# Kernel optimization log

Measured on AMD Instinct MI355X. Metric: run time of the kernel, lower is better.

Reference implementation:

```python
import jax, jax.numpy as jnp
import numpy as np

RC = 5.0          # cutoff radius (init arg rc)
N = 4096          # number of atoms
L = 40.0          # cubic box edge; rc <= 0.5*L so MIC branch is valid


def setup_inputs() -> dict:
    key = jax.random.key(0)
    coord = jax.random.uniform(key, (N, 3), dtype=jnp.float32) * L
    cell = L * jnp.eye(3, dtype=jnp.float32)
    return {"coord": coord, "cell": cell}


def reference(coord, cell):
    """MIC neighbor predicate, identical math to the torch cell-list MIC path.

    Returns:
      d2_masked: [n, n] float32, squared distance where pair is a neighbor
                 (0 < dist2 < rc^2), else 0. Row i, col j corresponds to the
                 directed pair (i, j) the torch module would emit in ind_2.
      shift:     [n, n, 3] int32 MIC lattice shift for each kept pair, 0 elsewhere.
    """
    rc2 = jnp.float32(RC * RC)
    H_inv = jnp.linalg.inv(cell)
    frac = coord @ H_inv
    frac = frac - jnp.floor(frac)                    # wrap into [0,1)
    # dfrac[i, j] = frac[j] - frac[i]  (j - i, matching torch: dj_frac - di_frac)
    dfrac = frac[None, :, :] - frac[:, None, :]      # [n, n, 3]
    shift_f = -jnp.round(dfrac)                      # MIC shift (float, in {-1,0,1})
    dfrac = dfrac + shift_f
    d = dfrac @ cell                                 # Cartesian displacement [n, n, 3]
    dist2 = jnp.sum(d * d, axis=-1)                  # [n, n]
    keep = (dist2 > 0.0) & (dist2 < rc2)
    d2_masked = jnp.where(keep, dist2, jnp.float32(0.0))
    shift = jnp.where(keep[..., None], shift_f.astype(jnp.int32), 0)
    return d2_masked, shift
```

## Files before the change

### kernel.cpp

```cpp
#include <hip/hip_runtime.h>


constexpr int N_ATOMS = 4096;
constexpr float RC2 = 25.0f;

typedef float v3f __attribute__((ext_vector_type(3)));

__global__ __launch_bounds__(256) void cellnl_kernel(
    const float* __restrict__ coord,
    const float* __restrict__ cell,
    float* __restrict__ out)
{
    const float L   = cell[0];
    const float inv = 1.0f / L;

    const int i = blockIdx.x >> 4;
    const int j = ((blockIdx.x & 15) << 8) + threadIdx.x;

    float fix = coord[3 * i + 0] * inv; fix -= floorf(fix);
    float fiy = coord[3 * i + 1] * inv; fiy -= floorf(fiy);
    float fiz = coord[3 * i + 2] * inv; fiz -= floorf(fiz);

    const v3f cjv = *reinterpret_cast<const v3f*>(coord + 3 * j);
    float fjx = cjv.x * inv; fjx -= floorf(fjx);
    float fjy = cjv.y * inv; fjy -= floorf(fjy);
    float fjz = cjv.z * inv; fjz -= floorf(fjz);

    float dx = fjx - fix, dy = fjy - fiy, dz = fjz - fiz;
    const float sx = -rintf(dx), sy = -rintf(dy), sz = -rintf(dz);
    dx += sx; dy += sy; dz += sz;
    dx *= L; dy *= L; dz *= L;

    const float dist2 = dx * dx + dy * dy + dz * dz;
    const bool keep = (dist2 > 0.0f) && (dist2 < RC2);

    const size_t p = (size_t)i * N_ATOMS + j;

    out[p] = keep ? dist2 : 0.0f;

    v3f sv;
    sv.x = keep ? sx : 0.0f;
    sv.y = keep ? sy : 0.0f;
    sv.z = keep ? sz : 0.0f;
    *reinterpret_cast<v3f*>(out + (size_t)N_ATOMS * N_ATOMS + p * 3) = sv;
}

extern "C" void kernel_launch(void* const* d_in, const int* in_sizes, int n_in,
                              void* d_out, int out_size, void* d_ws, size_t ws_size,
                              hipStream_t stream) {
    const float* coord = (const float*)d_in[0];
    const float* cell  = (const float*)d_in[1];
    float* out = (float*)d_out;

    const int blocks = N_ATOMS * (N_ATOMS / 256);
    hipLaunchKernelGGL(cellnl_kernel, dim3(blocks), dim3(256), 0, stream,
                       coord, cell, out);
}
```

Baseline: 255.7 us.

## Process four pairs per thread with LDS-staged coalesced 16-byte nontemporal stores

Each block now handles one full row i, and each thread computes four consecutive j per iteration using 16-byte coordinate loads. Shift triples are staged through shared memory so that every thread writes aligned 16-byte chunks, and all output stores use nontemporal hints. The aim is to make the write-bound 256 MB output stream fully coalesced with wide stores and fewer blocks. In exchange it adds two barriers per iteration and 12 KB of LDS per block.

```diff
diff --git a/kernel.cpp b/kernel.cpp
--- a/kernel.cpp
+++ b/kernel.cpp
@@ -1,48 +1,76 @@
 #include <hip/hip_runtime.h>
 
 
-constexpr int N_ATOMS = 4096;
-constexpr float RC2 = 25.0f;
+constexpr int   N_ATOMS = 4096;
+constexpr float RC2     = 25.0f;
+constexpr int   TPB     = 256;
 
-typedef float v3f __attribute__((ext_vector_type(3)));
+typedef float v4f __attribute__((ext_vector_type(4)));
 
-__global__ __launch_bounds__(256) void cellnl_kernel(
+__global__ __launch_bounds__(TPB) void cellnl_kernel(
     const float* __restrict__ coord,
     const float* __restrict__ cell,
     float* __restrict__ out)
 {
+    __shared__ float smem[TPB * 12];
+
     const float L   = cell[0];
     const float inv = 1.0f / L;
-
-    const int i = blockIdx.x >> 4;
-    const int j = ((blockIdx.x & 15) << 8) + threadIdx.x;
+    const int   i   = blockIdx.x;
+    const int   t   = threadIdx.x;
 
     float fix = coord[3 * i + 0] * inv; fix -= floorf(fix);
     float fiy = coord[3 * i + 1] * inv; fiy -= floorf(fiy);
     float fiz = coord[3 * i + 2] * inv; fiz -= floorf(fiz);
 
-    const v3f cjv = *reinterpret_cast<const v3f*>(coord + 3 * j);
-    float fjx = cjv.x * inv; fjx -= floorf(fjx);
-    float fjy = cjv.y * inv; fjy -= floorf(fjy);
-    float fjz = cjv.z * inv; fjz -= floorf(fjz);
+    const size_t prow  = (size_t)i * N_ATOMS;
+    float* const d2row = out + prow;
+    float* const shrow = out + (size_t)N_ATOMS * N_ATOMS + prow * 3;
 
-    float dx = fjx - fix, dy = fjy - fiy, dz = fjz - fiz;
-    const float sx = -rintf(dx), sy = -rintf(dy), sz = -rintf(dz);
-    dx += sx; dy += sy; dz += sz;
-    dx *= L; dy *= L; dz *= L;
+    #pragma unroll 1
+    for (int c = 0; c < 4; ++c) {
+        const int j0 = (c << 10) + (t << 2);
 
-    const float dist2 = dx * dx + dy * dy + dz * dz;
-    const bool keep = (dist2 > 0.0f) && (dist2 < RC2);
+        const v4f* cj = reinterpret_cast<const v4f*>(coord + 3 * j0);
+        const v4f c0 = cj[0], c1 = cj[1], c2 = cj[2];
+        const float cx[4] = {c0[0], c0[3], c1[2], c2[1]};
+        const float cy[4] = {c0[1], c1[0], c1[3], c2[2]};
+        const float cz[4] = {c0[2], c1[1], c2[0], c2[3]};
 
-    const size_t p = (size_t)i * N_ATOMS + j;
+        v4f   d2v;
+        float sv[12];
+        #pragma unroll
+        for (int p = 0; p < 4; ++p) {
+            float fjx = cx[p] * inv; fjx -= floorf(fjx);
+            float fjy = cy[p] * inv; fjy -= floorf(fjy);
+            float fjz = cz[p] * inv; fjz -= floorf(fjz);
+            float dx = fjx - fix, dy = fjy - fiy, dz = fjz - fiz;
+            const float sx = -rintf(dx), sy = -rintf(dy), sz = -rintf(dz);
+            dx = (dx + sx) * L; dy = (dy + sy) * L; dz = (dz + sz) * L;
+            const float dist2 = dx * dx + dy * dy + dz * dz;
+            const bool  keep  = (dist2 > 0.0f) && (dist2 < RC2);
+            d2v[p]      = keep ? dist2 : 0.0f;
+            sv[p*3 + 0] = keep ? sx : 0.0f;
+            sv[p*3 + 1] = keep ? sy : 0.0f;
+            sv[p*3 + 2] = keep ? sz : 0.0f;
+        }
 
-    out[p] = keep ? dist2 : 0.0f;
+        __builtin_nontemporal_store(d2v, reinterpret_cast<v4f*>(d2row + j0));
 
-    v3f sv;
-    sv.x = keep ? sx : 0.0f;
-    sv.y = keep ? sy : 0.0f;
-    sv.z = keep ? sz : 0.0f;
-    *reinterpret_cast<v3f*>(out + (size_t)N_ATOMS * N_ATOMS + p * 3) = sv;
+        #pragma unroll
+        for (int k = 0; k < 3; ++k) {
+            v4f w = { sv[4*k + 0], sv[4*k + 1], sv[4*k + 2], sv[4*k + 3] };
+            *reinterpret_cast<v4f*>(&smem[t * 12 + k * 4]) = w;
+        }
+        __syncthreads();
+        #pragma unroll
+        for (int k = 0; k < 3; ++k) {
+            const v4f v = *reinterpret_cast<const v4f*>(&smem[k * 1024 + t * 4]);
+            __builtin_nontemporal_store(
+                v, reinterpret_cast<v4f*>(shrow + c * 3072 + k * 1024 + t * 4));
+        }
+        __syncthreads();
+    }
 }
 
 extern "C" void kernel_launch(void* const* d_in, const int* in_sizes, int n_in,
@@ -52,7 +80,6 @@
     const float* cell  = (const float*)d_in[1];
     float* out = (float*)d_out;
 
-    const int blocks = N_ATOMS * (N_ATOMS / 256);
-    hipLaunchKernelGGL(cellnl_kernel, dim3(blocks), dim3(256), 0, stream,
+    hipLaunchKernelGGL(cellnl_kernel, dim3(N_ATOMS), dim3(TPB), 0, stream,
                        coord, cell, out);
 }
```

New measurement: 268.4 us. 5.0% more time.

## Split output into vectorized zero-fill plus sparse writes of kept pairs

Applied to the files above, without the earlier changes.

A separate kernel now zero-fills the whole output buffer with aligned 16-byte vector stores. The pair kernel then writes only the neighbor pairs that pass the cutoff, and writes their shift only when the shift is nonzero. The aim is to replace the dense, unaligned 12-byte shift stores across the full n×n×3 array with streaming aligned stores plus a small scattered write set. The cost is a second kernel launch, and the divergent, uncoalesced writes for the pairs that are kept.

```diff
diff --git a/kernel.cpp b/kernel.cpp
--- a/kernel.cpp
+++ b/kernel.cpp
@@ -1,12 +1,22 @@
 #include <hip/hip_runtime.h>
 
 
-constexpr int N_ATOMS = 4096;
-constexpr float RC2 = 25.0f;
+constexpr int   N_ATOMS = 4096;
+constexpr float RC2     = 25.0f;
 
 typedef float v3f __attribute__((ext_vector_type(3)));
+typedef float v4f __attribute__((ext_vector_type(4)));
 
-__global__ __launch_bounds__(256) void cellnl_kernel(
+__global__ __launch_bounds__(256) void zero_kernel(v4f* __restrict__ out)
+{
+    const int base = blockIdx.x * (256 * 16) + threadIdx.x;
+    #pragma unroll
+    for (int k = 0; k < 16; ++k) {
+        out[base + k * 256] = (v4f){0.0f, 0.0f, 0.0f, 0.0f};
+    }
+}
+
+__global__ __launch_bounds__(256) void pairs_kernel(
     const float* __restrict__ coord,
     const float* __restrict__ cell,
     float* __restrict__ out)
@@ -28,21 +38,20 @@
 
     float dx = fjx - fix, dy = fjy - fiy, dz = fjz - fiz;
     const float sx = -rintf(dx), sy = -rintf(dy), sz = -rintf(dz);
-    dx += sx; dy += sy; dz += sz;
-    dx *= L; dy *= L; dz *= L;
+    dx = (dx + sx) * L; dy = (dy + sy) * L; dz = (dz + sz) * L;
 
     const float dist2 = dx * dx + dy * dy + dz * dz;
-    const bool keep = (dist2 > 0.0f) && (dist2 < RC2);
+    const bool  keep  = (dist2 > 0.0f) && (dist2 < RC2);
 
-    const size_t p = (size_t)i * N_ATOMS + j;
-
-    out[p] = keep ? dist2 : 0.0f;
-
-    v3f sv;
-    sv.x = keep ? sx : 0.0f;
-    sv.y = keep ? sy : 0.0f;
-    sv.z = keep ? sz : 0.0f;
-    *reinterpret_cast<v3f*>(out + (size_t)N_ATOMS * N_ATOMS + p * 3) = sv;
+    if (keep) {
+        const size_t p = (size_t)i * N_ATOMS + j;
+        out[p] = dist2;
+        if ((sx != 0.0f) | (sy != 0.0f) | (sz != 0.0f)) {
+            v3f sv; sv.x = sx; sv.y = sy; sv.z = sz;
+            *reinterpret_cast<v3f*>(
+                out + (size_t)N_ATOMS * N_ATOMS + p * 3) = sv;
+        }
+    }
 }
 
 extern "C" void kernel_launch(void* const* d_in, const int* in_sizes, int n_in,
@@ -52,7 +61,9 @@
     const float* cell  = (const float*)d_in[1];
     float* out = (float*)d_out;
 
-    const int blocks = N_ATOMS * (N_ATOMS / 256);
-    hipLaunchKernelGGL(cellnl_kernel, dim3(blocks), dim3(256), 0, stream,
-                       coord, cell, out);
+    hipLaunchKernelGGL(zero_kernel, dim3(4096), dim3(256), 0, stream,
+                       (v4f*)out);
+
+    hipLaunchKernelGGL(pairs_kernel, dim3(N_ATOMS * (N_ATOMS / 256)), dim3(256),
+                       0, stream, coord, cell, out);
 }
```

After: 278.4 us. +8.9%, slower.
